# Kernel optimization log

Measured on AMD Instinct MI355X. Metric: run time of the kernel, lower is better.

## Reference

```python
import jax, jax.numpy as jnp
import numpy as np

B, S, D = 4, 2048, 1024
D_K, D_V = 1024, 1024


def setup_inputs() -> dict:
    key = jax.random.key(0)
    ks = jax.random.split(key, 9)
    s = 1.0 / np.sqrt(D)
    return {
        "q_in": jax.random.normal(ks[0], (B, S, D), jnp.float32),
        "k_in": jax.random.normal(ks[1], (B, S, D), jnp.float32),
        "v_in": jax.random.normal(ks[2], (B, S, D), jnp.float32),
        "Wq": jax.random.normal(ks[3], (D, D_K), jnp.float32) * s,
        "bq": jnp.zeros((D_K,), jnp.float32),
        "Wk": jax.random.normal(ks[4], (D, D_K), jnp.float32) * s,
        "bk": jnp.zeros((D_K,), jnp.float32),
        "Wv": jax.random.normal(ks[5], (D, D_V), jnp.float32) * s,
        "bv": jnp.zeros((D_V,), jnp.float32),
    }


def reference(q_in, k_in, v_in, Wq, bq, Wk, bk, Wv, bv):
    q = jnp.einsum("bsd,dk->bsk", q_in, Wq) + bq  # [B,S,d_k]
    k = jnp.einsum("bsd,dk->bsk", k_in, Wk) + bk  # [B,S,d_k]
    v = jnp.einsum("bsd,dv->bsv", v_in, Wv) + bv  # [B,S,d_v]
    scores = jnp.einsum("bqk,bsk->bqs", q, k) / jnp.sqrt(jnp.float32(D_K))
    attn = jax.nn.softmax(scores, axis=-1)  # [B,S,S]
    return jnp.einsum("bqs,bsv->bqv", attn, v)
```

## Files before the change

kernel.cpp:

```cpp
#include <hip/hip_runtime.h>
#include <stdint.h>

#define B_  4
#define S_  2048
#define D_  1024
#define DK_ 1024
#define DV_ 1024

typedef __attribute__((ext_vector_type(8)))  short short8;
typedef __attribute__((ext_vector_type(16))) float floatx16;

#define ASYNC16(gsrc, ldst)                                                        \
  __builtin_amdgcn_global_load_lds(                                                \
      (const __attribute__((address_space(1))) unsigned int*)(gsrc),               \
      (__attribute__((address_space(3))) unsigned int*)(ldst), 16, 0, 0)

#define WAITVM(N) asm volatile("s_waitcnt vmcnt(" #N ")" ::: "memory")

__device__ __forceinline__ unsigned short f2bf(float f) {
  union { float f; uint32_t u; } v; v.f = f;
  uint32_t r = v.u + 0x7fffu + ((v.u >> 16) & 1u);
  return (unsigned short)(r >> 16);
}

__global__ __launch_bounds__(256)
void prep(const float* __restrict__ q, const float* __restrict__ k, const float* __restrict__ v,
          const float* __restrict__ W0, const float* __restrict__ W1, const float* __restrict__ W2,
          unsigned short* __restrict__ qkv, unsigned short* __restrict__ WT) {
  const int bid = blockIdx.x, tid = threadIdx.x;
  if (bid < 12288) {
    const int t  = bid >> 12;
    const int cb = bid & 4095;
    const float* in = (t == 0) ? q : (t == 1) ? k : v;
    unsigned short* o = qkv + (long)t * ((long)B_ * S_ * D_);
    const int i0 = cb * 512 + tid;
    float4 v0 = ((const float4*)in)[i0];
    float4 v1 = ((const float4*)in)[i0 + 256];
    ushort4 u0, u1;
    u0.x = f2bf(v0.x); u0.y = f2bf(v0.y); u0.z = f2bf(v0.z); u0.w = f2bf(v0.w);
    u1.x = f2bf(v1.x); u1.y = f2bf(v1.y); u1.z = f2bf(v1.z); u1.w = f2bf(v1.w);
    ((ushort4*)o)[i0] = u0;
    ((ushort4*)o)[i0 + 256] = u1;
  } else {
    const int b2 = bid - 12288;
    const int w  = b2 >> 10;
    const int tl = b2 & 1023;
    const float* in = (w == 0) ? W0 : (w == 1) ? W1 : W2;
    unsigned short* o = WT + (long)w * D_ * DK_;
    __shared__ float tile[32][33];
    const int bx = (tl & 31) * 32, by = (tl >> 5) * 32;
    const int tx = tid & 31, ty = tid >> 5;
    for (int r = ty; r < 32; r += 8)
      tile[r][tx] = in[(long)(by + r) * DK_ + bx + tx];
    __syncthreads();
    for (int r = ty; r < 32; r += 8)
      o[(long)(bx + r) * D_ + by + tx] = f2bf(tile[tx][r]);
  }
}

__device__ __forceinline__ void storeC(float* p, float v)          { *p = v; }
__device__ __forceinline__ void storeC(unsigned short* p, float v) { *p = f2bf(v); }

__global__ __launch_bounds__(256)
void combine(float* __restrict__ out, const float* __restrict__ P,
             const float* __restrict__ rsp) {
  __shared__ float sinv;
  const int row = blockIdx.x;
  const int tid = threadIdx.x;
  if (tid < 32) {
    float s = rsp[(long)tid * (B_ * S_) + row];
#pragma unroll
    for (int m = 1; m < 32; m <<= 1) s += __shfl_xor(s, m, 64);
    if (tid == 0) sinv = 1.0f / s;
  }
  __syncthreads();
  const float inv = sinv;
  const long k = (long)row * 256 + tid;
  float4 a = ((const float4*)out)[k];
  float4 b = ((const float4*)P)[k];
  float4 o;
  o.x = (a.x + b.x) * inv; o.y = (a.y + b.y) * inv;
  o.z = (a.z + b.z) * inv; o.w = (a.w + b.w) * inv;
  ((float4*)out)[k] = o;
}

template <typename OutT, int NOUT, int MODE, int KSPL, int BM>
__global__ __launch_bounds__(512, 2)
void gemm_bt256(const unsigned short* __restrict__ A0, const unsigned short* __restrict__ A1,
                const unsigned short* __restrict__ A2, const unsigned short* __restrict__ Bm,
                OutT* __restrict__ C0, OutT* __restrict__ C1, OutT* __restrict__ C2,
                const float* __restrict__ b0, const float* __restrict__ b1,
                const float* __restrict__ b2, float* __restrict__ rsp,
                int N, int K, int lda, int ldb, long sA, long sB, long sC, float scale) {
  constexpr int IR = BM / 64;
  constexpr int IH = IR / 2;
  constexpr int nA = BM / 128;
  __shared__ __align__(16) unsigned short As[4][BM * 32];
  __shared__ __align__(16) unsigned short Bs[4][256 * 32];
  const int tid  = threadIdx.x;
  const int lane = tid & 63, wave = tid >> 6;
  const int wm = (wave >> 2) * (BM / 2);
  const int wn = (wave & 3) * 64;
  const int lm = lane & 31;
  const int hi = lane >> 5;

  const int gx = gridDim.x, gy = gridDim.y;
  const int T  = gx * gy * (int)gridDim.z;
  const int l  = blockIdx.x + gx * (blockIdx.y + gy * blockIdx.z);
  const int l2 = (l & 7) * (T >> 3) + (l >> 3);
  const int bxi = l2 % gx;
  const int byi = (l2 / gx) % gy;
  const int bzi = l2 / (gx * gy);

  const int  kh = (KSPL > 1) ? (bzi & (KSPL - 1)) : 0;
  const long zb = (KSPL > 1) ? (bzi >> 1) : bzi;
  const int m0  = byi * BM;
  const int n0g = bxi * 256;

  const unsigned short* A = A0;
  OutT* C = C0;
  const float* bias = b0;
  int n0 = n0g, sel = 0;
  if (NOUT == 3) {
    sel = n0g >> 10;
    n0 = n0g & 1023;
    if (sel == 1)      { A = A1; C = C1; bias = b1; }
    else if (sel == 2) { A = A2; C = C2; bias = b2; }
  }
  if (KSPL > 1 && kh) C = C1;
  A += zb * sA + (long)kh * K;
  const unsigned short* Bp = Bm + zb * sB + (long)kh * K;
  C += zb * sC;

  const int rr = lane >> 2;
  const int cc = (((lane & 3) ^ ((lane >> 3) & 3)) * 8);
  const unsigned short* gA0 = A  + (long)(m0  + (BM / 8) * wave + rr) * lda + cc;
  const unsigned short* gA1 = gA0 + 16 * (long)lda;
  const unsigned short* gB0 = Bp + (long)(n0g + 32 * wave + rr) * ldb + cc;
  const unsigned short* gB1 = gB0 + 16 * (long)ldb;
  const int aoff = wave * (BM * 4);
  const int boff = wave * 1024;

  floatx16 acc[IR][2] = {};
  const int sw = (lm >> 1) & 3;

  const int nt = K >> 5;

#pragma unroll
  for (int pt = 0; pt < 3; pt++) {
    ASYNC16(gA0, &As[pt][aoff]);
    if (nA == 2) ASYNC16(gA1, &As[pt][aoff + 512]);
    ASYNC16(gB0, &Bs[pt][boff]); ASYNC16(gB1, &Bs[pt][boff + 512]);
    gA0 += 32; gA1 += 32; gB0 += 32; gB1 += 32;
  }
  if constexpr (BM == 256) { WAITVM(8); } else { WAITVM(6); }
  __builtin_amdgcn_s_barrier();

  for (int t = 0; t < nt; t++) {
    const int bc = t & 3;
    const int bs = (t + 3) & 3;
    const bool pre = (t + 3 < nt);

    short8 af[IH][2], bf[2][2];
#pragma unroll
    for (int i = 0; i < IH; i++)
#pragma unroll
      for (int s = 0; s < 2; s++)
        af[i][s] = *(const short8*)&As[bc][(wm + i * 32 + lm) * 32 + (((s * 2 + hi) ^ sw) * 8)];
#pragma unroll
    for (int j = 0; j < 2; j++)
#pragma unroll
      for (int s = 0; s < 2; s++)
        bf[j][s] = *(const short8*)&Bs[bc][(wn + j * 32 + lm) * 32 + (((s * 2 + hi) ^ sw) * 8)];
    if (pre) {
      ASYNC16(gA0, &As[bs][aoff]);
      if (nA == 2) ASYNC16(gA1, &As[bs][aoff + 512]);
      gA0 += 32; gA1 += 32;
    }
    __builtin_amdgcn_s_barrier();
    asm volatile("s_waitcnt lgkmcnt(0)" ::: "memory");
    __builtin_amdgcn_s_setprio(1);
#pragma unroll
    for (int s = 0; s < 2; s++)
#pragma unroll
      for (int i = 0; i < IH; i++)
#pragma unroll
        for (int j = 0; j < 2; j++)
          acc[i][j] = __builtin_amdgcn_mfma_f32_32x32x16_bf16(af[i][s], bf[j][s], acc[i][j], 0, 0, 0);
    __builtin_amdgcn_s_setprio(0);
    __builtin_amdgcn_s_barrier();

    short8 af2[IH][2];
#pragma unroll
    for (int i = 0; i < IH; i++)
#pragma unroll
      for (int s = 0; s < 2; s++)
        af2[i][s] = *(const short8*)&As[bc][(wm + (IH + i) * 32 + lm) * 32 + (((s * 2 + hi) ^ sw) * 8)];
    if (pre) {
      ASYNC16(gB0, &Bs[bs][boff]); ASYNC16(gB1, &Bs[bs][boff + 512]);
      gB0 += 32; gB1 += 32;
    }
    __builtin_amdgcn_s_barrier();
    asm volatile("s_waitcnt lgkmcnt(0)" ::: "memory");
    __builtin_amdgcn_s_setprio(1);
#pragma unroll
    for (int s = 0; s < 2; s++)
#pragma unroll
      for (int i = 0; i < IH; i++)
#pragma unroll
        for (int j = 0; j < 2; j++)
          acc[IH + i][j] = __builtin_amdgcn_mfma_f32_32x32x16_bf16(af2[i][s], bf[j][s], acc[IH + i][j], 0, 0, 0);
    __builtin_amdgcn_s_setprio(0);
    if (t + 3 < nt)      { if constexpr (BM == 256) { WAITVM(8); } else { WAITVM(6); } }
    else if (t + 2 < nt) { if constexpr (BM == 256) { WAITVM(4); } else { WAITVM(3); } }
    else                 { WAITVM(0); }
    __builtin_amdgcn_s_barrier();
  }

  if (NOUT == 3 && sel == 2) {
    unsigned short* Vt = (unsigned short*)C;
    const int b = m0 >> 11;
    const int sbase = (m0 & 2047);
#pragma unroll
    for (int i = 0; i < IR; i++) {
      const int srowb = sbase + wm + i * 32 + (hi << 2);
#pragma unroll
      for (int j = 0; j < 2; j++) {
        const int col = n0 + wn + j * 32 + lm;
        const float bv = bias[col];
        unsigned short* vp = Vt + ((long)b * DV_ + col) * S_ + srowb;
#pragma unroll
        for (int g = 0; g < 4; g++) {
          ushort4 u;
          u.x = f2bf(acc[i][j][4 * g + 0] + bv);
          u.y = f2bf(acc[i][j][4 * g + 1] + bv);
          u.z = f2bf(acc[i][j][4 * g + 2] + bv);
          u.w = f2bf(acc[i][j][4 * g + 3] + bv);
          *(ushort4*)(vp + 8 * g) = u;
        }
      }
    }
  } else if (MODE == 1) {
#pragma unroll
    for (int i = 0; i < IR; i++) {
#pragma unroll
      for (int r = 0; r < 16; r++) {
        const int row = m0 + wm + i * 32 + (r & 3) + ((r >> 2) << 3) + (hi << 2);
        float sum2 = 0.f;
#pragma unroll
        for (int j = 0; j < 2; j++) {
          const int col = n0 + wn + j * 32 + lm;
          float e = __expf(acc[i][j][r] * scale);
          storeC(C + (long)row * N + col, e);
          sum2 += e;
        }
#pragma unroll
        for (int msk = 1; msk < 32; msk <<= 1) sum2 += __shfl_xor(sum2, msk, 64);
        if ((lane & 31) == 0)
          rsp[(long)(bxi * 4 + (wave & 3)) * (B_ * S_) + zb * S_ + row] = sum2;
      }
    }
  } else {
#pragma unroll
    for (int i = 0; i < IR; i++) {
#pragma unroll
      for (int j = 0; j < 2; j++) {
        const int col = n0 + wn + j * 32 + lm;
        const float bv = bias ? bias[col] : 0.f;
#pragma unroll
        for (int r = 0; r < 16; r++) {
          const int rl = wm + i * 32 + (r & 3) + ((r >> 2) << 3) + (hi << 2);
          storeC(C + (long)(m0 + rl) * N + col, acc[i][j][r] * scale + bv);
        }
      }
    }
  }
}

extern "C" void kernel_launch(void* const* d_in, const int* in_sizes, int n_in,
                              void* d_out, int out_size, void* d_ws, size_t ws_size,
                              hipStream_t stream) {
  const float* q_in = (const float*)d_in[0];
  const float* k_in = (const float*)d_in[1];
  const float* v_in = (const float*)d_in[2];
  const float* Wq   = (const float*)d_in[3];
  const float* bq   = (const float*)d_in[4];
  const float* Wk   = (const float*)d_in[5];
  const float* bk   = (const float*)d_in[6];
  const float* Wv   = (const float*)d_in[7];
  const float* bv   = (const float*)d_in[8];
  float* out = (float*)d_out;

  char* ws = (char*)d_ws;
  const long nX = (long)B_ * S_ * D_;
  const long nW = (long)D_ * DK_;
  unsigned short* qb  = (unsigned short*)(ws);
  unsigned short* kb  = qb + nX;
  unsigned short* vb  = kb + nX;
  unsigned short* WqT = vb + nX;
  unsigned short* Qb  = WqT + 3 * nW;
  unsigned short* Kb  = Qb + nX;
  unsigned short* Vt  = Kb + nX;
  unsigned short* U   = (unsigned short*)ws;
  float*          rowsumP = (float*)vb;
  float*          P   = (float*)Qb;

  dim3 blk(256), blk5(512);

  {
    dim3 g(12288 + 3072);
    prep<<<g, blk, 0, stream>>>(q_in, k_in, v_in, Wq, Wk, Wv, qb, WqT);
  }
  {
    dim3 g(3 * DK_ / 256, (B_ * S_) / 128, 1);
    gemm_bt256<unsigned short, 3, 0, 1, 128><<<g, blk5, 0, stream>>>(
        qb, kb, vb, WqT, Qb, Kb, Vt, bq, bk, bv, nullptr,
        DK_, D_, D_, D_, 0, 0, 0, 1.f);
  }
  {
    dim3 g(S_ / 256, S_ / 256, B_);
    gemm_bt256<unsigned short, 1, 1, 1, 256><<<g, blk5, 0, stream>>>(
        Qb, nullptr, nullptr, Kb, U, nullptr, nullptr, nullptr, nullptr, nullptr, rowsumP,
        S_, DK_, DK_, DK_, (long)S_ * DK_, (long)S_ * DK_, (long)S_ * S_, 0.03125f);
  }
  {
    dim3 g(DV_ / 256, S_ / 256, B_ * 2);
    gemm_bt256<float, 1, 0, 2, 256><<<g, blk5, 0, stream>>>(
        U, nullptr, nullptr, Vt, out, P, nullptr, nullptr, nullptr, nullptr, nullptr,
        DV_, S_ / 2, S_, S_, (long)S_ * S_, (long)DV_ * S_, (long)S_ * DV_, 1.f);
  }
  {
    dim3 g(B_ * S_);
    combine<<<g, blk, 0, stream>>>(out, P, rowsumP);
  }
}
```

Baseline: 344.5 us.

## Collapse split-phase GEMM main loop into single phase and use BM=256 for projections

The main K-loop of the bf16 MFMA GEMM previously split each tile into two halves, each with its own barriers and LDS fragment loads, interleaving A and B prefetches between them. It now loads all A and B fragments at once, issues all prefetches together, and runs every MFMA for the tile in one block, dropping two barriers and two lgkmcnt waits per iteration. The QKV projection launch also moves from BM=128 to BM=256 tiles, halving its grid. The trade-off is higher register pressure from holding all A fragments live, fewer blocks for the projection GEMM, and relying on compiler scheduling instead of explicit phase interleaving.

```diff
diff --git a/kernel.cpp b/kernel.cpp
--- a/kernel.cpp
+++ b/kernel.cpp
@@ -93,7 +93,6 @@
                 const float* __restrict__ b2, float* __restrict__ rsp,
                 int N, int K, int lda, int ldb, long sA, long sB, long sC, float scale) {
   constexpr int IR = BM / 64;
-  constexpr int IH = IR / 2;
   constexpr int nA = BM / 128;
   __shared__ __align__(16) unsigned short As[4][BM * 32];
   __shared__ __align__(16) unsigned short Bs[4][256 * 32];
@@ -155,15 +154,16 @@
   }
   if constexpr (BM == 256) { WAITVM(8); } else { WAITVM(6); }
   __builtin_amdgcn_s_barrier();
+  asm volatile("" ::: "memory");
 
   for (int t = 0; t < nt; t++) {
     const int bc = t & 3;
     const int bs = (t + 3) & 3;
     const bool pre = (t + 3 < nt);
 
-    short8 af[IH][2], bf[2][2];
-#pragma unroll
-    for (int i = 0; i < IH; i++)
+    short8 af[IR][2], bf[2][2];
+#pragma unroll
+    for (int i = 0; i < IR; i++)
 #pragma unroll
       for (int s = 0; s < 2; s++)
         af[i][s] = *(const short8*)&As[bc][(wm + i * 32 + lm) * 32 + (((s * 2 + hi) ^ sw) * 8)];
@@ -172,49 +172,29 @@
 #pragma unroll
       for (int s = 0; s < 2; s++)
         bf[j][s] = *(const short8*)&Bs[bc][(wn + j * 32 + lm) * 32 + (((s * 2 + hi) ^ sw) * 8)];
+
     if (pre) {
       ASYNC16(gA0, &As[bs][aoff]);
       if (nA == 2) ASYNC16(gA1, &As[bs][aoff + 512]);
-      gA0 += 32; gA1 += 32;
+      ASYNC16(gB0, &Bs[bs][boff]); ASYNC16(gB1, &Bs[bs][boff + 512]);
+      gA0 += 32; gA1 += 32; gB0 += 32; gB1 += 32;
     }
-    __builtin_amdgcn_s_barrier();
-    asm volatile("s_waitcnt lgkmcnt(0)" ::: "memory");
+
     __builtin_amdgcn_s_setprio(1);
 #pragma unroll
     for (int s = 0; s < 2; s++)
 #pragma unroll
-      for (int i = 0; i < IH; i++)
+      for (int i = 0; i < IR; i++)
 #pragma unroll
         for (int j = 0; j < 2; j++)
           acc[i][j] = __builtin_amdgcn_mfma_f32_32x32x16_bf16(af[i][s], bf[j][s], acc[i][j], 0, 0, 0);
     __builtin_amdgcn_s_setprio(0);
-    __builtin_amdgcn_s_barrier();
-
-    short8 af2[IH][2];
-#pragma unroll
-    for (int i = 0; i < IH; i++)
-#pragma unroll
-      for (int s = 0; s < 2; s++)
-        af2[i][s] = *(const short8*)&As[bc][(wm + (IH + i) * 32 + lm) * 32 + (((s * 2 + hi) ^ sw) * 8)];
-    if (pre) {
-      ASYNC16(gB0, &Bs[bs][boff]); ASYNC16(gB1, &Bs[bs][boff + 512]);
-      gB0 += 32; gB1 += 32;
-    }
-    __builtin_amdgcn_s_barrier();
-    asm volatile("s_waitcnt lgkmcnt(0)" ::: "memory");
-    __builtin_amdgcn_s_setprio(1);
-#pragma unroll
-    for (int s = 0; s < 2; s++)
-#pragma unroll
-      for (int i = 0; i < IH; i++)
-#pragma unroll
-        for (int j = 0; j < 2; j++)
-          acc[IH + i][j] = __builtin_amdgcn_mfma_f32_32x32x16_bf16(af2[i][s], bf[j][s], acc[IH + i][j], 0, 0, 0);
-    __builtin_amdgcn_s_setprio(0);
+
     if (t + 3 < nt)      { if constexpr (BM == 256) { WAITVM(8); } else { WAITVM(6); } }
     else if (t + 2 < nt) { if constexpr (BM == 256) { WAITVM(4); } else { WAITVM(3); } }
     else                 { WAITVM(0); }
     __builtin_amdgcn_s_barrier();
+    asm volatile("" ::: "memory");
   }
 
   if (NOUT == 3 && sel == 2) {
@@ -312,8 +292,8 @@
     prep<<<g, blk, 0, stream>>>(q_in, k_in, v_in, Wq, Wk, Wv, qb, WqT);
   }
   {
-    dim3 g(3 * DK_ / 256, (B_ * S_) / 128, 1);
-    gemm_bt256<unsigned short, 3, 0, 1, 128><<<g, blk5, 0, stream>>>(
+    dim3 g(3 * DK_ / 256, (B_ * S_) / 256, 1);
+    gemm_bt256<unsigned short, 3, 0, 1, 256><<<g, blk5, 0, stream>>>(
         qb, kb, vb, WqT, Qb, Kb, Vt, bq, bk, bv, nullptr,
         DK_, D_, D_, D_, 0, 0, 0, 1.f);
   }
```

After: 336.3 us. 1.02x faster.
